# Performance work log

Measured on AMD Instinct MI355X. Metric: run time of the kernel, lower is better.

Reference implementation:

```python
import jax, jax.numpy as jnp
import numpy as np

B, I, H, E, V, T = 512, 2560, 512, 300, 8000, 16
SOS = 2

def setup_inputs() -> dict:
    key = jax.random.key(0)
    ks = jax.random.split(key, 12)
    s = lambda k, shape: (jax.random.normal(k, shape, jnp.float32) * 0.05)
    emb = s(ks[2], (V, E)).at[0].set(0.0)  # padding_idx=0
    return dict(
        fused_features=jax.random.normal(ks[0], (B, I), jnp.float32),
        target_answers=jax.random.randint(ks[1], (B, T), 0, V),
        max_len=T,
        embedding=emb,
        W_in=s(ks[3], (H, I)), b_in=jnp.zeros((H,), jnp.float32),
        W_cell=s(ks[4], (H, I)), b_cell=jnp.zeros((H,), jnp.float32),
        W_ih0=s(ks[5], (4 * H, E + H)), W_hh0=s(ks[6], (4 * H, H)),
        b_ih0=jnp.zeros((4 * H,), jnp.float32), b_hh0=jnp.zeros((4 * H,), jnp.float32),
        W_ih1=s(ks[7], (4 * H, H)), W_hh1=s(ks[8], (4 * H, H)),
        b_ih1=jnp.zeros((4 * H,), jnp.float32), b_hh1=jnp.zeros((4 * H,), jnp.float32),
        W_out=s(ks[9], (V, H)), b_out=jnp.zeros((V,), jnp.float32),
    )

def _cell(gates, c):
    # PyTorch LSTM gate order: i, f, g, o
    i, f, g, o = jnp.split(gates, 4, axis=-1)
    c_new = jax.nn.sigmoid(f) * c + jax.nn.sigmoid(i) * jnp.tanh(g)
    h_new = jax.nn.sigmoid(o) * jnp.tanh(c_new)
    return h_new, c_new

def reference(fused_features, target_answers, max_len, embedding,
              W_in, b_in, W_cell, b_cell,
              W_ih0, W_hh0, b_ih0, b_hh0,
              W_ih1, W_hh1, b_ih1, b_hh1,
              W_out, b_out):
    context = fused_features @ W_in.T + b_in          # [B,H]
    cell0 = fused_features @ W_cell.T + b_cell        # [B,H]
    # teacher forcing (ratio=1.0, deterministic): inputs = [SOS, y_0..y_{T-2}]
    words = jnp.concatenate(
        [jnp.full((context.shape[0], 1), SOS, target_answers.dtype),
         target_answers[:, :-1]], axis=1)             # [B,T]
    emb = embedding[words]                            # [B,T,E]
    x = jnp.concatenate(
        [emb, jnp.broadcast_to(context[:, None, :], (emb.shape[0], emb.shape[1], context.shape[1]))],
        axis=-1)                                      # [B,T,E+H]
    # precompute input-side gates for layer 0 in one big GEMM
    xg0 = jnp.einsum('bti,gi->tbg', x, W_ih0) + b_ih0 + b_hh0  # [T,B,4H]

    def step(carry, xg):
        h0, c0, h1, c1 = carry
        h0, c0 = _cell(xg + h0 @ W_hh0.T, c0)
        h1, c1 = _cell(h0 @ W_ih1.T + b_ih1 + b_hh1 + h1 @ W_hh1.T, c1)
        return (h0, c0, h1, c1), h1

    init = (context, cell0, context, cell0)
    _, hs = jax.lax.scan(step, init, xg0)             # hs: [T,B,H]
    logits = jnp.einsum('tbh,vh->btv', hs, W_out) + b_out  # [B,T,V]
    return logits
```

## Files before the change

kernel.cpp:

```cpp
#include <hip/hip_runtime.h>
#include <cstdint>

#define B_   512
#define I_   2560
#define H_   512
#define E_   300
#define EW   320
#define V_   8000
#define VPAD 8064
#define T_   16
#define G4H  2048
#define SOS_ 2

typedef _Float16 f16;
typedef _Float16 f16x8 __attribute__((ext_vector_type(8)));
typedef _Float16 f16x4 __attribute__((ext_vector_type(4)));
typedef float    f32x4 __attribute__((ext_vector_type(4)));

__device__ __forceinline__ float sigmoidf_(float x) {
    return 1.0f / (1.0f + __expf(-x));
}

__device__ __forceinline__ void gload16(const void* g, void* l) {
    __builtin_amdgcn_global_load_lds(
        (const __attribute__((address_space(1))) void*)g,
        (__attribute__((address_space(3))) void*)l,
        16, 0, 0);
}

__global__ __launch_bounds__(256)
void gemm_mfma(const f16* __restrict__ A, int lda,
               const f16* __restrict__ Bw, int ldb,
               float* __restrict__ C, int ldc,
               int K, int Nvalid,
               const float* __restrict__ bias1)
{
    __shared__ f16 As[128][32];
    __shared__ f16 Bs[128][32];

    const int tid  = threadIdx.x;
    const int w    = tid >> 6;
    const int lane = tid & 63;
    const int bm   = blockIdx.x * 128;
    const int bn   = blockIdx.y * 128;
    const int wr   = w >> 1;
    const int wc   = w & 1;

    const int srow = lane >> 2;
    const int skel = (lane & 3) * 8;

    const f16* Ag0 = A  + (size_t)(bm + w*32 +      srow) * lda + skel;
    const f16* Ag1 = A  + (size_t)(bm + w*32 + 16 + srow) * lda + skel;
    const f16* Bg0 = Bw + (size_t)(bn + w*32 +      srow) * ldb + skel;
    const f16* Bg1 = Bw + (size_t)(bn + w*32 + 16 + srow) * ldb + skel;
    f16* Al0 = &As[w*32     ][0];
    f16* Al1 = &As[w*32 + 16][0];
    f16* Bl0 = &Bs[w*32     ][0];
    f16* Bl1 = &Bs[w*32 + 16][0];

    const int frow = lane & 15;
    const int fk   = (lane >> 4) * 8;

    f32x4 acc[4][4] = {};

    for (int k0 = 0; k0 < K; k0 += 32) {
        gload16(Ag0 + k0, Al0);
        gload16(Ag1 + k0, Al1);
        gload16(Bg0 + k0, Bl0);
        gload16(Bg1 + k0, Bl1);
        __syncthreads();

        f16x8 af[4], bf[4];
        #pragma unroll
        for (int m = 0; m < 4; ++m)
            af[m] = *reinterpret_cast<const f16x8*>(&As[wr*64 + m*16 + frow][fk]);
        #pragma unroll
        for (int n = 0; n < 4; ++n)
            bf[n] = *reinterpret_cast<const f16x8*>(&Bs[wc*64 + n*16 + frow][fk]);

        #pragma unroll
        for (int m = 0; m < 4; ++m)
            #pragma unroll
            for (int n = 0; n < 4; ++n)
                acc[m][n] = __builtin_amdgcn_mfma_f32_16x16x32_f16(
                    af[m], bf[n], acc[m][n], 0, 0, 0);

        __syncthreads();
    }

    const int rowb = bm + wr*64 + (lane >> 4) * 4;
    #pragma unroll
    for (int n = 0; n < 4; ++n) {
        const int col = bn + wc*64 + n*16 + frow;
        if (col >= Nvalid) continue;
        const float badd = bias1 ? bias1[col] : 0.0f;
        #pragma unroll
        for (int m = 0; m < 4; ++m) {
            const int r0 = rowb + m*16;
            #pragma unroll
            for (int r = 0; r < 4; ++r)
                C[(size_t)(r0 + r) * ldc + col] = acc[m][n][r] + badd;
        }
    }
}

__global__ __launch_bounds__(256)
void gemm_ctx_init(const f16* __restrict__ A,
                   const f16* __restrict__ Bw,
                   const float* __restrict__ b_in,
                   const float* __restrict__ b_cell,
                   f16* __restrict__ ctx16,
                   f16* __restrict__ h0, f16* __restrict__ h1,
                   float* __restrict__ c0, float* __restrict__ c1)
{
    __shared__ f16 As[128][32];
    __shared__ f16 Bs[128][32];

    const int tid  = threadIdx.x;
    const int w    = tid >> 6;
    const int lane = tid & 63;
    const int bm   = blockIdx.x * 128;
    const int bn   = blockIdx.y * 128;
    const int wr   = w >> 1;
    const int wc   = w & 1;

    const int srow = lane >> 2;
    const int skel = (lane & 3) * 8;

    const f16* Ag0 = A  + (size_t)(bm + w*32 +      srow) * I_ + skel;
    const f16* Ag1 = A  + (size_t)(bm + w*32 + 16 + srow) * I_ + skel;
    const f16* Bg0 = Bw + (size_t)(bn + w*32 +      srow) * I_ + skel;
    const f16* Bg1 = Bw + (size_t)(bn + w*32 + 16 + srow) * I_ + skel;
    f16* Al0 = &As[w*32     ][0];
    f16* Al1 = &As[w*32 + 16][0];
    f16* Bl0 = &Bs[w*32     ][0];
    f16* Bl1 = &Bs[w*32 + 16][0];

    const int frow = lane & 15;
    const int fk   = (lane >> 4) * 8;

    f32x4 acc[4][4] = {};

    for (int k0 = 0; k0 < I_; k0 += 32) {
        gload16(Ag0 + k0, Al0);
        gload16(Ag1 + k0, Al1);
        gload16(Bg0 + k0, Bl0);
        gload16(Bg1 + k0, Bl1);
        __syncthreads();

        f16x8 af[4], bf[4];
        #pragma unroll
        for (int m = 0; m < 4; ++m)
            af[m] = *reinterpret_cast<const f16x8*>(&As[wr*64 + m*16 + frow][fk]);
        #pragma unroll
        for (int n = 0; n < 4; ++n)
            bf[n] = *reinterpret_cast<const f16x8*>(&Bs[wc*64 + n*16 + frow][fk]);

        #pragma unroll
        for (int m = 0; m < 4; ++m)
            #pragma unroll
            for (int n = 0; n < 4; ++n)
                acc[m][n] = __builtin_amdgcn_mfma_f32_16x16x32_f16(
                    af[m], bf[n], acc[m][n], 0, 0, 0);

        __syncthreads();
    }

    const int rowb = bm + wr*64 + (lane >> 4) * 4;
    #pragma unroll
    for (int n = 0; n < 4; ++n) {
        const int col = bn + wc*64 + n*16 + frow;
        #pragma unroll
        for (int m = 0; m < 4; ++m) {
            const int r0 = rowb + m*16;
            #pragma unroll
            for (int r = 0; r < 4; ++r) {
                const int row = r0 + r;
                if (col < 512) {
                    const f16 ch = (f16)(acc[m][n][r] + b_in[col]);
                    ctx16[(size_t)row * 512 + col] = ch;
                    h0[(size_t)row * 512 + col] = ch;
                    h1[(size_t)row * 512 + col] = ch;
                } else {
                    const float cc = acc[m][n][r] + b_cell[col - 512];
                    c0[(size_t)row * 512 + col - 512] = cc;
                    c1[(size_t)row * 512 + col - 512] = cc;
                }
            }
        }
    }
}

__device__ __forceinline__ void gemm_cell_body(
    const f16* __restrict__ Ap1, const f16* __restrict__ Ap2, int lda2,
    const f16* __restrict__ Wp, int K,
    const float* __restrict__ Cadd,
    const float* __restrict__ bih, const float* __restrict__ bhh,
    float* __restrict__ cst,
    f16* __restrict__ hout1,
    char* smem, int bm, int bn)
{
    const int tid  = threadIdx.x;
    const int w    = tid >> 6;
    const int lane = tid & 63;
    const int wr   = w >> 1, wc = w & 1;
    const int frow = lane & 15, hi = lane >> 4;
    const int sw   = (frow & 7) << 4;
    const int srow8 = lane >> 3;
    const int ksb  = ((((lane & 7) * 16) ^ (srow8 << 4)) >> 1);

    const int NT = K >> 6;
    f32x4 acc[2][4] = {};

    char* Abuf = smem;
    char* Wbuf = smem + 16384;

    auto stage = [&](int bsel, int kt) {
        const int k0 = kt << 6;
        #pragma unroll
        for (int j = 0; j < 2; ++j) {
            const int row = w*16 + j*8 + srow8;
            const f16* src;
            if (k0 < 512) src = Ap1 + (size_t)(bm + row) * 512  + k0 + ksb;
            else          src = Ap2 + (size_t)(bm + row) * lda2 + (k0 - 512) + ksb;
            gload16(src, Abuf + bsel*8192 + (w*2 + j)*1024 + lane*16);
        }
        #pragma unroll
        for (int j = 0; j < 4; ++j) {
            const int row = w*32 + j*8 + srow8;
            gload16(Wp + (size_t)(bn + row) * K + k0 + ksb,
                    Wbuf + bsel*16384 + (w*4 + j)*1024 + lane*16);
        }
    };

    stage(0, 0);
    stage(1, 1);

    int buf = 0;
    for (int kt = 0; kt < NT; ++kt) {
        if (kt < NT - 1) asm volatile("s_waitcnt vmcnt(6)" ::: "memory");
        else             asm volatile("s_waitcnt vmcnt(0)" ::: "memory");
        __builtin_amdgcn_sched_barrier(0);
        __builtin_amdgcn_s_barrier();
        __builtin_amdgcn_sched_barrier(0);

        const char* A_ = Abuf + buf*8192;
        const char* W_ = Wbuf + buf*16384;
        f16x8 af[2][2], bf[2][4];
        #pragma unroll
        for (int ks = 0; ks < 2; ++ks) {
            const int cb = (ks*64 + hi*16) ^ sw;
            #pragma unroll
            for (int m = 0; m < 2; ++m)
                af[ks][m] = *reinterpret_cast<const f16x8*>(A_ + (wr*32 + m*16 + frow)*128 + cb);
            #pragma unroll
            for (int n = 0; n < 4; ++n)
                bf[ks][n] = *reinterpret_cast<const f16x8*>(W_ + (wc*64 + n*16 + frow)*128 + cb);
        }
        __builtin_amdgcn_sched_barrier(0);
        asm volatile("s_waitcnt lgkmcnt(0)" ::: "memory");
        __builtin_amdgcn_sched_barrier(0);
        __builtin_amdgcn_s_barrier();
        __builtin_amdgcn_sched_barrier(0);

        if (kt + 2 < NT) stage(buf, kt + 2);

        #pragma unroll
        for (int ks = 0; ks < 2; ++ks)
            #pragma unroll
            for (int m = 0; m < 2; ++m)
                #pragma unroll
                for (int n = 0; n < 4; ++n)
                    acc[m][n] = __builtin_amdgcn_mfma_f32_16x16x32_f16(
                        af[ks][m], bf[ks][n], acc[m][n], 0, 0, 0);
        buf ^= 1;
    }

    float* gs = (float*)smem;
    #pragma unroll
    for (int m = 0; m < 2; ++m) {
        const int row = wr*32 + m*16 + hi*4;
        #pragma unroll
        for (int n = 0; n < 4; ++n) {
            const int col = wc*64 + n*16 + frow;
            #pragma unroll
            for (int r = 0; r < 4; ++r) {
                float v = acc[m][n][r];
                if (Cadd) v += Cadd[(size_t)(bm + row + r) * G4H + bn + col];
                gs[(row + r)*132 + col] = v;
            }
        }
    }
    __syncthreads();

    const int hp = tid & 31;
    const int hg = (bn >> 2) + hp;
    float bi0 = 0.f, bi1 = 0.f, bi2 = 0.f, bi3 = 0.f;
    if (bih) {
        bi0 = bih[hg]        + bhh[hg];
        bi1 = bih[512 + hg]  + bhh[512 + hg];
        bi2 = bih[1024 + hg] + bhh[1024 + hg];
        bi3 = bih[1536 + hg] + bhh[1536 + hg];
    }
    #pragma unroll
    for (int i = 0; i < 8; ++i) {
        const int r = (tid >> 5) * 8 + i;
        const int b = bm + r;
        const float gi = gs[r*132 +      hp] + bi0;
        const float gf = gs[r*132 + 32 + hp] + bi1;
        const float gc = gs[r*132 + 64 + hp] + bi2;
        const float go = gs[r*132 + 96 + hp] + bi3;
        const float c  = cst[(size_t)b * 512 + hg];
        const float cn = sigmoidf_(gf) * c + sigmoidf_(gi) * tanhf(gc);
        const float hn = sigmoidf_(go) * tanhf(cn);
        cst[(size_t)b * 512 + hg] = cn;
        hout1[(size_t)b * 512 + hg] = (f16)hn;
    }
}

__device__ __forceinline__ void gemm_out_body(
    const f16* __restrict__ A, const f16* __restrict__ Bw,
    float* __restrict__ C,
    const float* __restrict__ bias,
    int bm, int bn, char* smem, int tid)
{
    const int w    = tid >> 6;
    const int lane = tid & 63;
    const int wr   = w >> 1, wc = w & 1;
    const int frow = lane & 15, hi = lane >> 4;
    const int sw   = (frow & 7) << 4;
    const int srow8 = lane >> 3;
    const int ksb  = ((((lane & 7) * 16) ^ (srow8 << 4)) >> 1);

    char* Abuf = smem;
    char* Wbuf = smem + 32768;
    f32x4 acc[4][4] = {};

    auto stage = [&](int bsel, int kt) {
        const int k0 = kt << 6;
        #pragma unroll
        for (int j = 0; j < 4; ++j) {
            const int row = w*32 + j*8 + srow8;
            gload16(A  + (size_t)(bm + row) * 512 + k0 + ksb,
                    Abuf + bsel*16384 + (w*4 + j)*1024 + lane*16);
            gload16(Bw + (size_t)(bn + row) * 512 + k0 + ksb,
                    Wbuf + bsel*16384 + (w*4 + j)*1024 + lane*16);
        }
    };

    stage(0, 0);
    stage(1, 1);

    int buf = 0;
    for (int kt = 0; kt < 8; ++kt) {
        if (kt < 7) asm volatile("s_waitcnt vmcnt(8)" ::: "memory");
        else        asm volatile("s_waitcnt vmcnt(0)" ::: "memory");
        __builtin_amdgcn_sched_barrier(0);
        __builtin_amdgcn_s_barrier();
        __builtin_amdgcn_sched_barrier(0);

        const char* A_ = Abuf + buf*16384;
        const char* W_ = Wbuf + buf*16384;
        f16x8 af[2][4], bf[2][4];
        #pragma unroll
        for (int ks = 0; ks < 2; ++ks) {
            const int cb = (ks*64 + hi*16) ^ sw;
            #pragma unroll
            for (int m = 0; m < 4; ++m)
                af[ks][m] = *reinterpret_cast<const f16x8*>(A_ + (wr*64 + m*16 + frow)*128 + cb);
            #pragma unroll
            for (int n = 0; n < 4; ++n)
                bf[ks][n] = *reinterpret_cast<const f16x8*>(W_ + (wc*64 + n*16 + frow)*128 + cb);
        }
        __builtin_amdgcn_sched_barrier(0);
        asm volatile("s_waitcnt lgkmcnt(0)" ::: "memory");
        __builtin_amdgcn_sched_barrier(0);
        __builtin_amdgcn_s_barrier();
        __builtin_amdgcn_sched_barrier(0);

        if (kt + 2 < 8) stage(buf, kt + 2);

        #pragma unroll
        for (int ks = 0; ks < 2; ++ks)
            #pragma unroll
            for (int m = 0; m < 4; ++m)
                #pragma unroll
                for (int n = 0; n < 4; ++n)
                    acc[m][n] = __builtin_amdgcn_mfma_f32_16x16x32_f16(
                        af[ks][m], bf[ks][n], acc[m][n], 0, 0, 0);
        buf ^= 1;
    }

    const int rowb = bm + wr*64 + (lane >> 4) * 4;
    #pragma unroll
    for (int n = 0; n < 4; ++n) {
        const int col = bn + wc*64 + n*16 + frow;
        if (col >= V_) continue;
        const float badd = bias[col];
        #pragma unroll
        for (int m = 0; m < 4; ++m) {
            const int r0 = rowb + m*16;
            #pragma unroll
            for (int r = 0; r < 4; ++r)
                __builtin_nontemporal_store(
                    acc[m][n][r] + badd,
                    &C[(size_t)(r0 + r) * (T_ * V_) + col]);
        }
    }
}

__global__ __launch_bounds__(256)
void phase_kernel(const f16* __restrict__ h0in,
                  const f16* __restrict__ embt,
                  f16* __restrict__ h0out,
                  const f16* __restrict__ h1in,
                  f16* __restrict__ h1out,
                  const f16* __restrict__ W0p, const f16* __restrict__ W1p,
                  const f16* __restrict__ WoutP,
                  const float* __restrict__ ctxg,
                  const float* __restrict__ bih1, const float* __restrict__ bhh1,
                  const float* __restrict__ b_out,
                  float* __restrict__ c0, float* __restrict__ c1,
                  float* __restrict__ out, int tout,
                  int active0, int active1, int activeO)
{
    __shared__ char smem[65536];
    const int bx = blockIdx.x;

    if (bx < 128) {
        if (!active0) return;
        const int xcd = bx & 7, idx = bx >> 3;
        const int bn = (xcd*2 + (idx & 1)) * 128;
        const int bm = (idx >> 1) * 64;
        gemm_cell_body(h0in, embt, EW, W0p, 832,
                       ctxg, nullptr, nullptr, c0, h0out, smem, bm, bn);
    } else if (bx < 256) {
        if (!active1) return;
        const int lb = bx - 128;
        const int xcd = lb & 7, idx = lb >> 3;
        const int bn = (xcd*2 + (idx & 1)) * 128;
        const int bm = (idx >> 1) * 64;
        gemm_cell_body(h0in, h1in, 512, W1p, 1024,
                       nullptr, bih1, bhh1, c1, h1out, smem, bm, bn);
    } else {
        if (!activeO) return;
        const int o = bx - 256;
        const int xcd = o & 7, j = o >> 3;
        const int bnt = xcd*8 + (j >> 2);
        if (bnt >= 63) return;
        const int bm = (j & 3) * 128;
        gemm_out_body(h1in, WoutP, out + (size_t)tout * V_, b_out,
                      bm, bnt * 128, smem, threadIdx.x);
    }
}

#define NB_F16   1280
#define NB_WIC   2560
#define NB_W0    6656
#define NB_W1    8192
#define NB_WCTX  4096
#define NB_B0    8
#define NB_WOUT  4032
#define NB_EMB   10240
#define NB_TOTAL (NB_F16+NB_WIC+NB_W0+NB_W1+NB_WCTX+NB_B0+NB_WOUT+NB_EMB)

__global__ __launch_bounds__(256)
void pack_all(const float* __restrict__ fused,
              const float* __restrict__ Win, const float* __restrict__ Wcell,
              const float* __restrict__ Whh0, const float* __restrict__ Wih0,
              const float* __restrict__ Wih1, const float* __restrict__ Whh1,
              const float* __restrict__ bih0, const float* __restrict__ bhh0,
              const float* __restrict__ Wout,
              const float* __restrict__ emb, const int* __restrict__ target,
              f16* __restrict__ fused16, f16* __restrict__ WinCell,
              f16* __restrict__ W0, f16* __restrict__ W1,
              f16* __restrict__ Wc, float* __restrict__ b01p,
              f16* __restrict__ Wo, f16* __restrict__ embAll)
{
    int bx = blockIdx.x;
    const int tid = threadIdx.x;

    if (bx < NB_F16) {
        const int i = bx * 256 + tid;
        const float4 v = reinterpret_cast<const float4*>(fused)[i];
        f16x4 h = { (f16)v.x, (f16)v.y, (f16)v.z, (f16)v.w };
        *reinterpret_cast<f16x4*>(fused16 + (size_t)i * 4) = h;
        return;
    }
    bx -= NB_F16;
    if (bx < NB_WIC) {
        const int i = bx * 256 + tid;
        const int r = i / 640, c4 = (i % 640) * 4;
        const float* src = (r < 512) ? Win + (size_t)r * I_ + c4
                                     : Wcell + (size_t)(r - 512) * I_ + c4;
        const float4 v = *reinterpret_cast<const float4*>(src);
        f16x4 h = { (f16)v.x, (f16)v.y, (f16)v.z, (f16)v.w };
        *reinterpret_cast<f16x4*>(WinCell + (size_t)i * 4) = h;
        return;
    }
    bx -= NB_WIC;
    if (bx < NB_W0) {
        const int idx = bx * 256 + tid;
        const int rp = idx / 832, k = idx % 832;
        const int g = (rp >> 5) & 3, h = (rp >> 7) * 32 + (rp & 31);
        const int srow = g * 512 + h;
        float v;
        if (k < 512)      v = Whh0[(size_t)srow * 512 + k];
        else if (k < 812) v = Wih0[(size_t)srow * 812 + (k - 512)];
        else              v = 0.0f;
        W0[idx] = (f16)v;
        return;
    }
    bx -= NB_W0;
    if (bx < NB_W1) {
        const int idx = bx * 256 + tid;
        const int rp = idx >> 10, k = idx & 1023;
        const int g = (rp >> 5) & 3, h = (rp >> 7) * 32 + (rp & 31);
        const int srow = g * 512 + h;
        const float v = (k < 512) ? Wih1[(size_t)srow * 512 + k]
                                  : Whh1[(size_t)srow * 512 + (k - 512)];
        W1[idx] = (f16)v;
        return;
    }
    bx -= NB_W1;
    if (bx < NB_WCTX) {
        const int idx = bx * 256 + tid;
        const int rp = idx >> 9, k = idx & 511;
        const int g = (rp >> 5) & 3, h = (rp >> 7) * 32 + (rp & 31);
        Wc[idx] = (f16)Wih0[(size_t)(g * 512 + h) * 812 + 300 + k];
        return;
    }
    bx -= NB_WCTX;
    if (bx < NB_B0) {
        const int idx = bx * 256 + tid;
        const int g = (idx >> 5) & 3, h = (idx >> 7) * 32 + (idx & 31);
        b01p[idx] = bih0[g * 512 + h] + bhh0[g * 512 + h];
        return;
    }
    bx -= NB_B0;
    if (bx < NB_WOUT) {
        const int i = bx * 256 + tid;
        const int r = i >> 7, c4 = (i & 127) * 4;
        f16x4 h = { (f16)0.f, (f16)0.f, (f16)0.f, (f16)0.f };
        if (r < V_) {
            const float4 v = *reinterpret_cast<const float4*>(Wout + (size_t)r * H_ + c4);
            h = f16x4{ (f16)v.x, (f16)v.y, (f16)v.z, (f16)v.w };
        }
        *reinterpret_cast<f16x4*>(Wo + (size_t)i * 4) = h;
        return;
    }
    bx -= NB_WOUT;
    {
        const int idx = bx * 256 + tid;
        const int t = idx / (B_ * EW);
        const int rem = idx % (B_ * EW);
        const int b = rem / EW, e = rem % EW;
        const int wd = (t == 0) ? SOS_ : target[b * T_ + (t - 1)];
        const float v = (e < E_) ? emb[(size_t)wd * E_ + e] : 0.0f;
        embAll[idx] = (f16)v;
    }
}

extern "C" void kernel_launch(void* const* d_in, const int* in_sizes, int n_in,
                              void* d_out, int out_size, void* d_ws, size_t ws_size,
                              hipStream_t stream)
{
    const float* fused  = (const float*)d_in[0];
    const int*   target = (const int*)d_in[1];
    const float* emb    = (const float*)d_in[3];
    const float* W_in   = (const float*)d_in[4];
    const float* b_in   = (const float*)d_in[5];
    const float* W_cell = (const float*)d_in[6];
    const float* b_cell = (const float*)d_in[7];
    const float* W_ih0  = (const float*)d_in[8];
    const float* W_hh0  = (const float*)d_in[9];
    const float* b_ih0  = (const float*)d_in[10];
    const float* b_hh0  = (const float*)d_in[11];
    const float* W_ih1  = (const float*)d_in[12];
    const float* W_hh1  = (const float*)d_in[13];
    const float* b_ih1  = (const float*)d_in[14];
    const float* b_hh1  = (const float*)d_in[15];
    const float* W_out  = (const float*)d_in[16];
    const float* b_out  = (const float*)d_in[17];
    float* out = (float*)d_out;

    char* p = (char*)d_ws;
    auto carve = [&](size_t bytes) {
        char* r = p;
        p += (bytes + 255) & ~(size_t)255;
        return r;
    };
    float* ctxg   = (float*)carve((size_t)B_ * G4H * 4);
    float* b01p   = (float*)carve((size_t)G4H * 4);
    float* c0     = (float*)carve((size_t)B_ * H_ * 4);
    float* c1     = (float*)carve((size_t)B_ * H_ * 4);
    f16* fused16  = (f16*)carve((size_t)B_ * I_ * 2);
    f16* WinCell  = (f16*)carve((size_t)1024 * I_ * 2);
    f16* W0p      = (f16*)carve((size_t)G4H * 832 * 2);
    f16* W1p      = (f16*)carve((size_t)G4H * 1024 * 2);
    f16* Wctxp    = (f16*)carve((size_t)G4H * H_ * 2);
    f16* Wout16   = (f16*)carve((size_t)VPAD * H_ * 2);
    f16* ctx16    = (f16*)carve((size_t)B_ * H_ * 2);
    f16* h0a      = (f16*)carve((size_t)B_ * H_ * 2);
    f16* h0b      = (f16*)carve((size_t)B_ * H_ * 2);
    f16* h1a      = (f16*)carve((size_t)B_ * H_ * 2);
    f16* h1b      = (f16*)carve((size_t)B_ * H_ * 2);
    f16* embAll   = (f16*)carve((size_t)T_ * B_ * EW * 2);

    pack_all<<<dim3(NB_TOTAL), 256, 0, stream>>>(
        fused, W_in, W_cell, W_hh0, W_ih0, W_ih1, W_hh1,
        b_ih0, b_hh0, W_out, emb, target,
        fused16, WinCell, W0p, W1p, Wctxp, b01p, Wout16, embAll);

    gemm_ctx_init<<<dim3(B_/128, 1024/128), 256, 0, stream>>>(
        fused16, WinCell, b_in, b_cell, ctx16, h0b, h1b, c0, c1);

    gemm_mfma<<<dim3(B_/128, G4H/128), 256, 0, stream>>>(
        ctx16, H_, Wctxp, H_, ctxg, G4H, H_, G4H, b01p);

    f16* h0buf[2] = { h0a, h0b };
    f16* h1buf[2] = { h1a, h1b };
    for (int phase = 0; phase <= T_ + 1; ++phase) {
        const int a0 = (phase < T_) ? 1 : 0;
        const int a1 = (phase >= 1 && phase <= T_) ? 1 : 0;
        const int aO = (phase >= 2) ? 1 : 0;
        const int te = (phase < T_) ? phase : (T_ - 1);
        const int tO = aO ? (phase - 2) : 0;
        phase_kernel<<<dim3(512), 256, 0, stream>>>(
            h0buf[(phase + 1) & 1],
            embAll + (size_t)te * B_ * EW,
            h0buf[phase & 1],
            h1buf[phase & 1],
            h1buf[(phase + 1) & 1],
            W0p, W1p, Wout16, ctxg, b_ih1, b_hh1, b_out,
            c0, c1, out, tO, a0, a1, aO);
    }
}
```

Before: 447.2 us.

## Triple-buffer LSTM cell GEMM, store ctx gates in fp16, trim idle phase blocks

The cell GEMM prefetch goes from double to triple buffering: three K-tiles are in flight, with matching vmcnt waits, and shared memory grows to 72KB. The precomputed context gate term is now stored and read as fp16 instead of fp32, which halves its traffic in every layer-0 step at some cost in precision. Prologue and epilogue phases now launch only the blocks that have work, using a block offset, instead of launching 512 and letting inactive ones exit. The larger shared memory footprint may lower occupancy.

After: 417.6 us. 1.07x faster.

```diff
diff --git a/kernel.cpp b/kernel.cpp
--- a/kernel.cpp
+++ b/kernel.cpp
@@ -29,11 +29,11 @@
 }
 
 __global__ __launch_bounds__(256)
-void gemm_mfma(const f16* __restrict__ A, int lda,
-               const f16* __restrict__ Bw, int ldb,
-               float* __restrict__ C, int ldc,
-               int K, int Nvalid,
-               const float* __restrict__ bias1)
+void gemm_mfma_f16o(const f16* __restrict__ A, int lda,
+                    const f16* __restrict__ Bw, int ldb,
+                    f16* __restrict__ C, int ldc,
+                    int K,
+                    const float* __restrict__ bias1)
 {
     __shared__ f16 As[128][32];
     __shared__ f16 Bs[128][32];
@@ -92,14 +92,13 @@
     #pragma unroll
     for (int n = 0; n < 4; ++n) {
         const int col = bn + wc*64 + n*16 + frow;
-        if (col >= Nvalid) continue;
         const float badd = bias1 ? bias1[col] : 0.0f;
         #pragma unroll
         for (int m = 0; m < 4; ++m) {
             const int r0 = rowb + m*16;
             #pragma unroll
             for (int r = 0; r < 4; ++r)
-                C[(size_t)(r0 + r) * ldc + col] = acc[m][n][r] + badd;
+                C[(size_t)(r0 + r) * ldc + col] = (f16)(acc[m][n][r] + badd);
         }
     }
 }
@@ -194,7 +193,7 @@
 __device__ __forceinline__ void gemm_cell_body(
     const f16* __restrict__ Ap1, const f16* __restrict__ Ap2, int lda2,
     const f16* __restrict__ Wp, int K,
-    const float* __restrict__ Cadd,
+    const f16* __restrict__ Cadd,
     const float* __restrict__ bih, const float* __restrict__ bhh,
     float* __restrict__ cst,
     f16* __restrict__ hout1,
@@ -213,7 +212,7 @@
     f32x4 acc[2][4] = {};
 
     char* Abuf = smem;
-    char* Wbuf = smem + 16384;
+    char* Wbuf = smem + 24576;
 
     auto stage = [&](int bsel, int kt) {
         const int k0 = kt << 6;
@@ -235,11 +234,14 @@
 
     stage(0, 0);
     stage(1, 1);
+    stage(2, 2);
 
     int buf = 0;
     for (int kt = 0; kt < NT; ++kt) {
-        if (kt < NT - 1) asm volatile("s_waitcnt vmcnt(6)" ::: "memory");
-        else             asm volatile("s_waitcnt vmcnt(0)" ::: "memory");
+        const int rem = NT - 1 - kt;
+        if (rem >= 2)      asm volatile("s_waitcnt vmcnt(12)" ::: "memory");
+        else if (rem == 1) asm volatile("s_waitcnt vmcnt(6)" ::: "memory");
+        else               asm volatile("s_waitcnt vmcnt(0)" ::: "memory");
         __builtin_amdgcn_sched_barrier(0);
         __builtin_amdgcn_s_barrier();
         __builtin_amdgcn_sched_barrier(0);
@@ -263,7 +265,7 @@
         __builtin_amdgcn_s_barrier();
         __builtin_amdgcn_sched_barrier(0);
 
-        if (kt + 2 < NT) stage(buf, kt + 2);
+        if (kt + 3 < NT) stage(buf, kt + 3);
 
         #pragma unroll
         for (int ks = 0; ks < 2; ++ks)
@@ -273,7 +275,7 @@
                 for (int n = 0; n < 4; ++n)
                     acc[m][n] = __builtin_amdgcn_mfma_f32_16x16x32_f16(
                         af[ks][m], bf[ks][n], acc[m][n], 0, 0, 0);
-        buf ^= 1;
+        buf = (buf == 2) ? 0 : buf + 1;
     }
 
     float* gs = (float*)smem;
@@ -286,7 +288,7 @@
             #pragma unroll
             for (int r = 0; r < 4; ++r) {
                 float v = acc[m][n][r];
-                if (Cadd) v += Cadd[(size_t)(bm + row + r) * G4H + bn + col];
+                if (Cadd) v += (float)Cadd[(size_t)(bm + row + r) * G4H + bn + col];
                 gs[(row + r)*132 + col] = v;
             }
         }
@@ -417,15 +419,15 @@
                   f16* __restrict__ h1out,
                   const f16* __restrict__ W0p, const f16* __restrict__ W1p,
                   const f16* __restrict__ WoutP,
-                  const float* __restrict__ ctxg,
+                  const f16* __restrict__ ctxg,
                   const float* __restrict__ bih1, const float* __restrict__ bhh1,
                   const float* __restrict__ b_out,
                   float* __restrict__ c0, float* __restrict__ c1,
                   float* __restrict__ out, int tout,
-                  int active0, int active1, int activeO)
+                  int bx0, int active0, int active1, int activeO)
 {
-    __shared__ char smem[65536];
-    const int bx = blockIdx.x;
+    __shared__ char smem[73728];
+    const int bx = blockIdx.x + bx0;
 
     if (bx < 128) {
         if (!active0) return;
@@ -590,7 +592,7 @@
         p += (bytes + 255) & ~(size_t)255;
         return r;
     };
-    float* ctxg   = (float*)carve((size_t)B_ * G4H * 4);
+    f16* ctxg     = (f16*)carve((size_t)B_ * G4H * 2);
     float* b01p   = (float*)carve((size_t)G4H * 4);
     float* c0     = (float*)carve((size_t)B_ * H_ * 4);
     float* c1     = (float*)carve((size_t)B_ * H_ * 4);
@@ -615,8 +617,8 @@
     gemm_ctx_init<<<dim3(B_/128, 1024/128), 256, 0, stream>>>(
         fused16, WinCell, b_in, b_cell, ctx16, h0b, h1b, c0, c1);
 
-    gemm_mfma<<<dim3(B_/128, G4H/128), 256, 0, stream>>>(
-        ctx16, H_, Wctxp, H_, ctxg, G4H, H_, G4H, b01p);
+    gemm_mfma_f16o<<<dim3(B_/128, G4H/128), 256, 0, stream>>>(
+        ctx16, H_, Wctxp, H_, ctxg, G4H, H_, b01p);
 
     f16* h0buf[2] = { h0a, h0b };
     f16* h1buf[2] = { h1a, h1b };
@@ -626,13 +628,18 @@
         const int aO = (phase >= 2) ? 1 : 0;
         const int te = (phase < T_) ? phase : (T_ - 1);
         const int tO = aO ? (phase - 2) : 0;
-        phase_kernel<<<dim3(512), 256, 0, stream>>>(
+        int bx0 = 0, nb = 512;
+        if (phase == 0)            { bx0 = 0;   nb = 128; }
+        else if (phase == 1)       { bx0 = 0;   nb = 256; }
+        else if (phase == T_)      { bx0 = 128; nb = 384; }
+        else if (phase == T_ + 1)  { bx0 = 256; nb = 256; }
+        phase_kernel<<<dim3(nb), 256, 0, stream>>>(
             h0buf[(phase + 1) & 1],
             embAll + (size_t)te * B_ * EW,
             h0buf[phase & 1],
             h1buf[phase & 1],
             h1buf[(phase + 1) & 1],
             W0p, W1p, Wout16, ctxg, b_ih1, b_hh1, b_out,
-            c0, c1, out, tO, a0, a1, aO);
-    }
-}
+            c0, c1, out, tO, bx0, a0, a1, aO);
+    }
+}
```
